# Optimization experiments

Hardware: AMD Instinct MI355X
Metric: run time of the kernel (lower is better)

The kernel has to match this reference:

```python
import jax, jax.numpy as jnp
import numpy as np

# static config (mirrors params)
T, B, NA, NF = 48, 256, 23, 4
D = NA * NF          # y_dim = 92
XD = 2               # x_dim
H = 128              # rnn_dim
HD = 128             # h_dim
NL = 2               # n_layers
FS = 0.1
BURN = 12
IN_ENC = XD + D + H  # GRU input size = 222
A0, A1 = 12, 11      # agents 0..11 -> net0, 12..22 -> net1


def setup_inputs() -> dict:
    key = jax.random.key(0)
    ks = jax.random.split(key, 16)
    s = 0.05
    rn = lambda k, shape: jax.random.normal(k, shape, jnp.float32) * s
    return {
        "states": jax.random.normal(ks[0], (T + 1, 1, B, D), jnp.float32),
        # per-network (leading dim 2) GRU layer-0 and layer-1 weights (torch GRU layout: [r|z|n])
        "W_ih0": rn(ks[1], (2, 3 * H, IN_ENC)),
        "W_hh0": rn(ks[2], (2, 3 * H, H)),
        "b_ih0": rn(ks[3], (2, 3 * H)),
        "b_hh0": rn(ks[4], (2, 3 * H)),
        "W_ih1": rn(ks[5], (2, 3 * H, H)),
        "W_hh1": rn(ks[6], (2, 3 * H, H)),
        "b_ih1": rn(ks[7], (2, 3 * H)),
        "b_hh1": rn(ks[8], (2, 3 * H)),
        # decoder MLP (dropout is identity in eval) + mean head
        "W1": rn(ks[9], (2, HD, H)),
        "b1": rn(ks[10], (2, HD)),
        "W2": rn(ks[11], (2, HD, HD)),
        "b2": rn(ks[12], (2, HD)),
        "Wm": rn(ks[13], (2, XD, HD)),
        "bm": rn(ks[14], (2, XD)),
        "rollout": 0,
        "train": 0,
    }


def _gru_cell(x, h, Wih, Whh, bih, bhh):
    gi = x @ Wih.T + bih
    gh = h @ Whh.T + bhh
    r = jax.nn.sigmoid(gi[:, :H] + gh[:, :H])
    z = jax.nn.sigmoid(gi[:, H:2 * H] + gh[:, H:2 * H])
    n = jnp.tanh(gi[:, 2 * H:] + r * gh[:, 2 * H:])
    return (1.0 - z) * n + z * h


def _batch_error(a, b):
    # sum over batch of the euclidean norm over features
    return jnp.sum(jnp.sqrt(jnp.sum((a - b) ** 2, axis=1)))


def _group_step(h, y_t, y3, y3n, lo, hi, g, P):
    # h: [NL, A*B, H]; agents lo..hi-1 of network g, folded into the batch dim
    A = hi - lo
    vel = y3[:, lo:hi, 2:4].transpose(1, 0, 2).reshape(A * B, 2)
    pos = y3[:, lo:hi, 0:2].transpose(1, 0, 2).reshape(A * B, 2)
    vel_true = y3n[:, lo:hi, 2:4].transpose(1, 0, 2).reshape(A * B, 2)
    pos_true = y3n[:, lo:hi, 0:2].transpose(1, 0, 2).reshape(A * B, 2)
    y_rep = jnp.broadcast_to(y_t[None], (A, B, D)).reshape(A * B, D)
    h_last = h[-1]
    enc_in = jnp.concatenate([vel, y_rep, h_last], axis=1)  # [A*B, IN_ENC]
    # decoder uses the PRE-update hidden state
    d = jax.nn.relu(h_last @ P["W1"][g].T + P["b1"][g])
    d = jax.nn.relu(d @ P["W2"][g].T + P["b2"][g])
    dm = d @ P["Wm"][g].T + P["bm"][g]  # [A*B, XD]
    # 2-layer GRU step
    h0n = _gru_cell(enc_in, h[0], P["W_ih0"][g], P["W_hh0"][g], P["b_ih0"][g], P["b_hh0"][g])
    h1n = _gru_cell(h0n, h[1], P["W_ih1"][g], P["W_hh1"][g], P["b_ih1"][g], P["b_hh1"][g])
    h_new = jnp.stack([h0n, h1n])
    L = _batch_error(dm, vel_true)
    ep = _batch_error(pos + vel * FS, pos_true)
    ev = _batch_error(dm[:, :2], vel_true)
    return h_new, L, ep, ev


def _forward(states, P):
    y_seq = states[:T, 0]       # [T, B, D]
    y_next = states[1:T + 1, 0]  # [T, B, D]

    def step(carry, xs):
        h0, h1, L, ep, ev = carry
        y_t, y_t1, t = xs
        y3 = y_t.reshape(B, NA, NF)
        y3n = y_t1.reshape(B, NA, NF)
        h0n, L0, ep0, ev0 = _group_step(h0, y_t, y3, y3n, 0, A0, 0, P)
        h1n, L1, ep1, ev1 = _group_step(h1, y_t, y3, y3n, A0, NA, 1, P)
        m = (t >= BURN).astype(jnp.float32)
        return (h0n, h1n, L + L0 + L1, ep + m * (ep0 + ep1), ev + m * (ev0 + ev1)), None

    init = (jnp.zeros((NL, A0 * B, H), jnp.float32),
            jnp.zeros((NL, A1 * B, H), jnp.float32),
            jnp.zeros((), jnp.float32), jnp.zeros((), jnp.float32), jnp.zeros((), jnp.float32))
    (h0, h1, L, ep, ev), _ = jax.lax.scan(step, init, (y_seq, y_next, jnp.arange(T)))
    L_rec = L / (T * NA)
    e_pos = ep / ((T - BURN) * NA)
    e_vel = ev / ((T - BURN) * NA)
    return L_rec, e_pos, e_vel


def reference(states, W_ih0, W_hh0, b_ih0, b_hh0, W_ih1, W_hh1, b_ih1, b_hh1,
              W1, b1, W2, b2, Wm, bm, rollout, train):
    P = dict(W_ih0=W_ih0, W_hh0=W_hh0, b_ih0=b_ih0, b_hh0=b_hh0,
             W_ih1=W_ih1, W_hh1=W_hh1, b_ih1=b_ih1, b_hh1=b_hh1,
             W1=W1, b1=b1, W2=W2, b2=b2, Wm=Wm, bm=bm)
    return _forward(states, P)
```

## Files before the change

kernel.cpp:

```cpp
#include <hip/hip_runtime.h>
#include <hip/hip_bf16.h>


typedef unsigned short u16;
typedef unsigned int u32;
typedef unsigned char u8;
typedef __attribute__((ext_vector_type(4))) float f32x4;
typedef __attribute__((ext_vector_type(4))) int i32x4;
typedef __attribute__((ext_vector_type(8))) int i32x8;

#define MFMA128(acc, a, b) \
  (acc) = __builtin_amdgcn_mfma_scale_f32_16x16x128_f8f6f4( \
      (a), (b), (acc), 0, 0, 0, 0x7F7F7F7F, 0, 0x7F7F7F7F)

__device__ __forceinline__ i32x8 ld8(const u8* p) { return *(const i32x8*)p; }
__device__ __forceinline__ void pinV(i32x8& x) { asm volatile("" : "+v"(x)); }

__device__ __forceinline__ u8 f2e4(float v) {
  return (u8)(__builtin_amdgcn_cvt_pk_fp8_f32(v, 0.f, 0, false) & 0xff);
}
__device__ __forceinline__ u32 pk4(float a, float b, float c, float d) {
  u32 p = (u32)__builtin_amdgcn_cvt_pk_fp8_f32(a, b, 0, false);
  return (u32)__builtin_amdgcn_cvt_pk_fp8_f32(c, d, (int)p, true);
}
__device__ __forceinline__ float sigf(float x) {
  return __builtin_amdgcn_rcpf(1.f + __expf(-x));
}
__device__ __forceinline__ float tanh_fast(float x) {
  return 1.f - 2.f * __builtin_amdgcn_rcpf(1.f + __expf(2.f * x));
}

__device__ __forceinline__ int swzo(int row, int o) {
  return (row << 7) + ((((o >> 5) ^ row) & 3) << 5) +
         ((((o >> 4) ^ (row >> 2)) & 1) << 4) + (o & 15);
}
__device__ __forceinline__ i32x8 ldfrag(const u8* b, int row, int kq) {
  const int h = (row >> 2) & 1;
  const int a = (row << 7) + (((kq ^ row) & 3) << 5);
  i32x4 lo = *(const i32x4*)(b + a + (h << 4));
  i32x4 hi = *(const i32x4*)(b + a + ((h ^ 1) << 4));
  return __builtin_shufflevector(lo, hi, 0, 1, 2, 3, 4, 5, 6, 7);
}

constexpr int E0 = 2 * 384 * 352;
constexpr int E1 = E0 + 2 * 384 * 256;
constexpr int E2 = E1 + 2 * 128 * 128;
constexpr int E3 = E2 + 2 * 128 * 128;
constexpr int E4 = E3 + 2 * 128 * 128;
constexpr int E5 = E4 + 2 * 128 * 128;
constexpr int NBIAS = 2048;
constexpr int TOTAL = E5 + NBIAS + 4;
constexpr int WB_BYTE_OFF = 16384;

constexpr int WB0A_REL = E5;
constexpr int YBG2_REL = WB0A_REL + 23 * 384 * 128;
constexpr int NA1 = TOTAL;
constexpr int NA2 = NA1 + 23 * 384 * 128;
constexpr int NA3 = NA2 + 48 * 256 * 128;

__global__ void prep_kernel(const float* __restrict__ states,
                            const float* __restrict__ Wih0, const float* __restrict__ Whh0,
                            const float* __restrict__ bih0, const float* __restrict__ bhh0,
                            const float* __restrict__ Wih1, const float* __restrict__ Whh1,
                            const float* __restrict__ bih1, const float* __restrict__ bhh1,
                            const float* __restrict__ W1, const float* __restrict__ W2,
                            u8* __restrict__ wb, float* __restrict__ wsf) {
  for (int idx = blockIdx.x * blockDim.x + threadIdx.x; idx < NA3;
       idx += gridDim.x * blockDim.x) {
    if (idx < E0) {
      int g = idx / 135168;
      int r = idx - g * 135168;
      int j = r / 352;
      int k = r - j * 352;
      const float* wi = Wih0 + (g * 384 + j) * 222;
      float v;
      if (k < 94) v = wi[k];
      else if (k < 96) v = 0.f;
      else if (k < 224) v = wi[k - 2];
      else v = Whh0[(g * 384 + j) * 128 + (k - 224)];
      wb[idx] = f2e4(v);
    } else if (idx < E1) {
      int q = idx - E0;
      int g = q / 98304;
      int r = q - g * 98304;
      int j = r >> 8;
      int k = r & 255;
      float v = (k < 128) ? Wih1[(g * 384 + j) * 128 + k]
                          : Whh1[(g * 384 + j) * 128 + (k - 128)];
      wb[idx] = f2e4(v);
    } else if (idx < E2) {
      int q = idx - E1; int g = q >> 14; int r = q & 16383; int j = r >> 7; int k = r & 127;
      wb[idx] = f2e4(W1[(g * 128 + j) * 128 + k]);
    } else if (idx < E3) {
      int q = idx - E2; int g = q >> 14; int r = q & 16383; int j = r >> 7; int k = r & 127;
      wb[idx] = f2e4(W2[(g * 128 + j) * 128 + k]);
    } else if (idx < E5) {
      wb[idx] = 0;
    } else if (idx < E5 + NBIAS) {
      int q = idx - E5;
      float v;
      if (q < 512)       { int g = q >> 8, j = q & 255;              v = bih0[g*384 + j] + bhh0[g*384 + j]; }
      else if (q < 768)  { int p = q - 512;  int g = p >> 7, j = p & 127; v = bih0[g*384 + 256 + j]; }
      else if (q < 1024) { int p = q - 768;  int g = p >> 7, j = p & 127; v = bhh0[g*384 + 256 + j]; }
      else if (q < 1536) { int p = q - 1024; int g = p >> 8, j = p & 255; v = bih1[g*384 + j] + bhh1[g*384 + j]; }
      else if (q < 1792) { int p = q - 1536; int g = p >> 7, j = p & 127; v = bih1[g*384 + 256 + j]; }
      else               { int p = q - 1792; int g = p >> 7, j = p & 127; v = bhh1[g*384 + 256 + j]; }
      wsf[4 + q] = v;
    } else if (idx < TOTAL) {
      wsf[idx - (E5 + NBIAS)] = 0.f;
    } else if (idx < NA2) {
      int q = idx - NA1;
      int a = q / 49152;
      int r = q - a * 49152;
      int j = r >> 7;
      int k = r & 127;
      const float* wi = Wih0 + (((a >= 12) ? 1 : 0) * 384 + j) * 222;
      float v = (k < 92) ? wi[2 + k] : 0.f;
      if (k == a * 4 + 2) v += wi[0];
      if (k == a * 4 + 3) v += wi[1];
      wb[WB0A_REL + q] = f2e4(v);
    } else {
      int q = idx - NA2;
      int t = q >> 15;
      int r = q & 32767;
      int row = r >> 7;
      int k = r & 127;
      float v = (k < 92) ? states[((size_t)t * 256 + row) * 92 + k] : 0.f;
      wb[YBG2_REL + q] = f2e4(v);
    }
  }
}

__global__ __launch_bounds__(512, 2) __attribute__((amdgpu_waves_per_eu(2, 2)))
void rnn_kernel(const float* __restrict__ states,
                const u8* __restrict__ wb,
                float* __restrict__ wsf,
                const float* __restrict__ b1g,
                const float* __restrict__ b2g,
                const float* __restrict__ Wmg,
                const float* __restrict__ bmg) {
  const int blk = blockIdx.x;
  const int g = (blk < 96) ? 0 : 1;
  const int r0 = (g == 0) ? (blk * 32) : ((blk - 96) * 32);
  const int aAg = (g == 0 ? 0 : 12) + (r0 >> 8);
  const int b0 = r0 & 255;

  const int tid = threadIdx.x;
  const int wid = tid >> 6;
  const int ln = tid & 63;
  const int j_in = ln & 15;
  const int kq = ln >> 4;
  const int c0 = wid * 16 + kq * 4;
  const int jh = wid * 16 + j_in;

  __shared__ __align__(64) u8 h0b[2][32 * 128];
  __shared__ __align__(64) u8 h1b[2][32 * 128];
  __shared__ __align__(64) u8 d1b[32 * 128];
  __shared__ __align__(64) u8 d2b[32 * 128];
  __shared__ __align__(16) float bias[1536];
  __shared__ float dmv[48][32][2];
  __shared__ float red[8][3];

  const u8* W0   = wb + g * 135168;
  const u8* W1c  = wb + E0 + g * 98304;
  const u8* Wm1p = wb + E1 + g * 16384;
  const u8* Wm2p = wb + E2 + g * 16384;
  const u8* WB0A = wb + WB0A_REL + aAg * 49152;
  const u8* YBG  = wb + YBG2_REL;

  i32x8 w0r0 = ld8(WB0A + jh * 128 + kq * 32);
  i32x8 w0r1 = ld8(W0 + jh * 352 + 96 + kq * 32);
  i32x8 w0r2 = ld8(W0 + jh * 352 + 224 + kq * 32);
  i32x8 w0z0 = ld8(WB0A + (128 + jh) * 128 + kq * 32);
  i32x8 w0z1 = ld8(W0 + (128 + jh) * 352 + 96 + kq * 32);
  i32x8 w0z2 = ld8(W0 + (128 + jh) * 352 + 224 + kq * 32);
  i32x8 w0n0 = ld8(WB0A + (256 + jh) * 128 + kq * 32);
  i32x8 w0n1 = ld8(W0 + (256 + jh) * 352 + 96 + kq * 32);
  i32x8 wn0  = ld8(W0 + (256 + jh) * 352 + 224 + kq * 32);
  i32x8 w1r0 = ld8(W1c + jh * 256 + kq * 32);
  i32x8 w1r1 = ld8(W1c + jh * 256 + 128 + kq * 32);
  i32x8 w1z0 = ld8(W1c + (128 + jh) * 256 + kq * 32);
  i32x8 w1z1 = ld8(W1c + (128 + jh) * 256 + 128 + kq * 32);
  i32x8 w1n0 = ld8(W1c + (256 + jh) * 256 + kq * 32);
  i32x8 wn1  = ld8(W1c + (256 + jh) * 256 + 128 + kq * 32);
  i32x8 wm1  = ld8(Wm1p + jh * 128 + kq * 32);
  i32x8 wm2  = ld8(Wm2p + jh * 128 + kq * 32);
  pinV(w0r0); pinV(w0r1); pinV(w0r2);
  pinV(w0z0); pinV(w0z1); pinV(w0z2);
  pinV(w0n0); pinV(w0n1); pinV(wn0);
  pinV(w1r0); pinV(w1r1); pinV(w1z0); pinV(w1z1);
  pinV(w1n0); pinV(wn1); pinV(wm1); pinV(wm2);

  for (int i = tid; i < 1536; i += 512) {
    float v;
    if (i < 256)       v = wsf[4 + g * 256 + i];
    else if (i < 384)  v = wsf[516 + g * 128 + (i - 256)];
    else if (i < 512)  v = wsf[772 + g * 128 + (i - 384)];
    else if (i < 768)  v = wsf[1028 + g * 256 + (i - 512)];
    else if (i < 896)  v = wsf[1540 + g * 128 + (i - 768)];
    else if (i < 1024) v = wsf[1796 + g * 128 + (i - 896)];
    else if (i < 1152) v = b1g[g * 128 + (i - 1024)];
    else if (i < 1280) v = b2g[g * 128 + (i - 1152)];
    else               v = Wmg[g * 256 + (i - 1280)];
    bias[i] = v;
  }
  for (int i = tid; i < 32 * 128; i += 512) { h0b[0][i] = 0; h1b[0][i] = 0; }

  f32x4 hv0[2] = {{0,0,0,0},{0,0,0,0}};
  f32x4 hv1[2] = {{0,0,0,0},{0,0,0,0}};
  __syncthreads();

  for (int t = 0; t < 48; ++t) {
    const int cur = t & 1, nxt = cur ^ 1;
    const u8* h0c = h0b[cur]; u8* h0n = h0b[nxt];
    const u8* h1c = h1b[cur]; u8* h1n = h1b[nxt];
    const u8* yt = YBG + t * 32768;

    i32x8 fh1k[2];
    {
      f32x4 b1v = *(const f32x4*)(bias + 1024 + c0);
      f32x4 brv = *(const f32x4*)(bias + c0);
      f32x4 bzv = *(const f32x4*)(bias + 128 + c0);
      f32x4 biv = *(const f32x4*)(bias + 256 + c0);
      f32x4 bhv = *(const f32x4*)(bias + 384 + c0);
#pragma unroll
      for (int nt = 0; nt < 2; ++nt) {
        const int row = nt * 16 + j_in;
        i32x8 fy  = ld8(yt + (b0 + row) * 128 + kq * 32);
        i32x8 fh1 = ldfrag(h1c, row, kq);
        i32x8 fh0 = ldfrag(h0c, row, kq);
        fh1k[nt] = fh1;
        f32x4 mm = {0,0,0,0};
        MFMA128(mm, wm1, fh1);
        f32x4 aR = {0,0,0,0}, aZ = {0,0,0,0}, aN = {0,0,0,0}, aG = {0,0,0,0};
        MFMA128(aR, w0r0, fy);  MFMA128(aZ, w0z0, fy);  MFMA128(aN, w0n0, fy);
        MFMA128(aR, w0r1, fh1); MFMA128(aZ, w0z1, fh1); MFMA128(aN, w0n1, fh1);
        MFMA128(aR, w0r2, fh0); MFMA128(aZ, w0z2, fh0); MFMA128(aG, wn0, fh0);
        *(u32*)(d1b + swzo(row, c0)) =
          pk4(fmaxf(mm[0]+b1v[0],0.f), fmaxf(mm[1]+b1v[1],0.f),
              fmaxf(mm[2]+b1v[2],0.f), fmaxf(mm[3]+b1v[3],0.f));
#pragma unroll
        for (int i = 0; i < 4; ++i) {
          float rv = sigf(aR[i] + brv[i]);
          float zv = sigf(aZ[i] + bzv[i]);
          float nv = tanh_fast(aN[i] + biv[i] + rv * (aG[i] + bhv[i]));
          hv0[nt][i] = (1.f - zv) * nv + zv * hv0[nt][i];
        }
        *(u32*)(h0n + swzo(row, c0)) = pk4(hv0[nt][0], hv0[nt][1], hv0[nt][2], hv0[nt][3]);
      }
    }
    if (t > 0) {
      int row = tid >> 4, c = (tid >> 3) & 1, part = tid & 7;
      const float* wmr = bias + 1280 + c * 128 + part * 16;
      float s = 0.f;
#pragma unroll
      for (int q = 0; q < 4; ++q) {
        u32 w = *(const u32*)(d2b + swzo(row, part * 16 + q * 4));
        s += wmr[q * 4 + 0] * __builtin_amdgcn_cvt_f32_fp8((int)w, 0);
        s += wmr[q * 4 + 1] * __builtin_amdgcn_cvt_f32_fp8((int)w, 1);
        s += wmr[q * 4 + 2] * __builtin_amdgcn_cvt_f32_fp8((int)w, 2);
        s += wmr[q * 4 + 3] * __builtin_amdgcn_cvt_f32_fp8((int)w, 3);
      }
      s += __shfl_xor(s, 1); s += __shfl_xor(s, 2); s += __shfl_xor(s, 4);
      if (part == 0) dmv[t - 1][row][c] = s;
    }
    __syncthreads();

    {
      f32x4 b2v = *(const f32x4*)(bias + 1152 + c0);
      f32x4 brv = *(const f32x4*)(bias + 512 + c0);
      f32x4 bzv = *(const f32x4*)(bias + 640 + c0);
      f32x4 biv = *(const f32x4*)(bias + 768 + c0);
      f32x4 bhv = *(const f32x4*)(bias + 896 + c0);
#pragma unroll
      for (int nt = 0; nt < 2; ++nt) {
        const int row = nt * 16 + j_in;
        i32x8 fd1 = ldfrag(d1b, row, kq);
        i32x8 fg0 = ldfrag(h0n, row, kq);
        f32x4 mm = {0,0,0,0};
        MFMA128(mm, wm2, fd1);
        f32x4 aR = {0,0,0,0}, aZ = {0,0,0,0}, aN = {0,0,0,0}, aG = {0,0,0,0};
        MFMA128(aR, w1r0, fg0);      MFMA128(aZ, w1z0, fg0);      MFMA128(aN, w1n0, fg0);
        MFMA128(aR, w1r1, fh1k[nt]); MFMA128(aZ, w1z1, fh1k[nt]); MFMA128(aG, wn1, fh1k[nt]);
        *(u32*)(d2b + swzo(row, c0)) =
          pk4(fmaxf(mm[0]+b2v[0],0.f), fmaxf(mm[1]+b2v[1],0.f),
              fmaxf(mm[2]+b2v[2],0.f), fmaxf(mm[3]+b2v[3],0.f));
#pragma unroll
        for (int i = 0; i < 4; ++i) {
          float rv = sigf(aR[i] + brv[i]);
          float zv = sigf(aZ[i] + bzv[i]);
          float nv = tanh_fast(aN[i] + biv[i] + rv * (aG[i] + bhv[i]));
          hv1[nt][i] = (1.f - zv) * nv + zv * hv1[nt][i];
        }
        *(u32*)(h1n + swzo(row, c0)) = pk4(hv1[nt][0], hv1[nt][1], hv1[nt][2], hv1[nt][3]);
      }
    }
    __syncthreads();
  }

  {
    int row = tid >> 4, c = (tid >> 3) & 1, part = tid & 7;
    const float* wmr = bias + 1280 + c * 128 + part * 16;
    float s = 0.f;
#pragma unroll
    for (int q = 0; q < 4; ++q) {
      u32 w = *(const u32*)(d2b + swzo(row, part * 16 + q * 4));
      s += wmr[q * 4 + 0] * __builtin_amdgcn_cvt_f32_fp8((int)w, 0);
      s += wmr[q * 4 + 1] * __builtin_amdgcn_cvt_f32_fp8((int)w, 1);
      s += wmr[q * 4 + 2] * __builtin_amdgcn_cvt_f32_fp8((int)w, 2);
      s += wmr[q * 4 + 3] * __builtin_amdgcn_cvt_f32_fp8((int)w, 3);
    }
    s += __shfl_xor(s, 1); s += __shfl_xor(s, 2); s += __shfl_xor(s, 4);
    if (part == 0) dmv[47][row][c] = s;
  }
  __syncthreads();

  float accL = 0.f, accEp = 0.f, accEv = 0.f;
  const float bm0 = bmg[g * 2], bm1 = bmg[g * 2 + 1];
  for (int idx = tid; idx < 1536; idx += 512) {
    int t = idx >> 5, row = idx & 31;
    const float* sr = states + ((size_t)(t * 256 + b0 + row)) * 92 + aAg * 4;
    const float* sn = sr + 256 * 92;
    float dx = dmv[t][row][0] + bm0 - sn[2];
    float dy = dmv[t][row][1] + bm1 - sn[3];
    float e = sqrtf(dx * dx + dy * dy);
    accL += e;
    if (t >= 12) {
      accEv += e;
      float ex = sr[0] + 0.1f * sr[2] - sn[0];
      float ey = sr[1] + 0.1f * sr[3] - sn[1];
      accEp += sqrtf(ex * ex + ey * ey);
    }
  }
#pragma unroll
  for (int k = 1; k < 64; k <<= 1) {
    accL  += __shfl_xor(accL, k);
    accEp += __shfl_xor(accEp, k);
    accEv += __shfl_xor(accEv, k);
  }
  if (ln == 0) { red[wid][0] = accL; red[wid][1] = accEp; red[wid][2] = accEv; }
  __syncthreads();
  if (tid < 3) {
    float s = 0.f;
    for (int i = 0; i < 8; ++i) s += red[i][tid];
    atomicAdd(&wsf[tid], s);
  }
}

__global__ void fin_kernel(const float* __restrict__ wacc, float* __restrict__ out) {
  if (threadIdx.x == 0 && blockIdx.x == 0) {
    out[0] = wacc[0] / 1104.f;
    out[1] = wacc[1] / 828.f;
    out[2] = wacc[2] / 828.f;
  }
}

extern "C" void kernel_launch(void* const* d_in, const int* in_sizes, int n_in,
                              void* d_out, int out_size, void* d_ws, size_t ws_size,
                              hipStream_t stream) {
  const float* states = (const float*)d_in[0];
  const float* Wih0 = (const float*)d_in[1];
  const float* Whh0 = (const float*)d_in[2];
  const float* bih0 = (const float*)d_in[3];
  const float* bhh0 = (const float*)d_in[4];
  const float* Wih1 = (const float*)d_in[5];
  const float* Whh1 = (const float*)d_in[6];
  const float* bih1 = (const float*)d_in[7];
  const float* bhh1 = (const float*)d_in[8];
  const float* W1   = (const float*)d_in[9];
  const float* b1   = (const float*)d_in[10];
  const float* W2   = (const float*)d_in[11];
  const float* b2   = (const float*)d_in[12];
  const float* Wm   = (const float*)d_in[13];
  const float* bm   = (const float*)d_in[14];

  float* wsf = (float*)d_ws;
  u8* wb = (u8*)d_ws + WB_BYTE_OFF;

  int prep_blocks = (NA3 + 255) / 256;
  if (prep_blocks > 2048) prep_blocks = 2048;
  prep_kernel<<<prep_blocks, 256, 0, stream>>>(states, Wih0, Whh0, bih0, bhh0,
                                               Wih1, Whh1, bih1, bhh1,
                                               W1, W2, wb, wsf);
  rnn_kernel<<<184, 512, 0, stream>>>(states, wb, wsf, b1, b2, Wm, bm);
  fin_kernel<<<1, 64, 0, stream>>>(wsf, (float*)d_out);
}
```

Before: 274.9 us.

## Halve rows per block to double grid size for the sequential RNN

Each block now processes 16 batch rows instead of 32, so the grid doubles from 184 to 368 blocks and each wave handles one 16-row MFMA tile per step instead of two. The goal is to shorten the serial 48-step critical path per block and fill more CUs, because the recurrence cannot be parallelised over time. The cost is that every block reloads the full register-resident weight set, and with the occupancy hint raised to 4 waves per EU the register budget per thread shrinks, which may force spills. The decoder-head reduction and loss loop are re-indexed to match the 16-row tile.

```diff
diff --git a/kernel.cpp b/kernel.cpp
--- a/kernel.cpp
+++ b/kernel.cpp
@@ -131,7 +131,7 @@
   }
 }
 
-__global__ __launch_bounds__(512, 2) __attribute__((amdgpu_waves_per_eu(2, 2)))
+__global__ __launch_bounds__(512) __attribute__((amdgpu_waves_per_eu(4, 4)))
 void rnn_kernel(const float* __restrict__ states,
                 const u8* __restrict__ wb,
                 float* __restrict__ wsf,
@@ -140,8 +140,8 @@
                 const float* __restrict__ Wmg,
                 const float* __restrict__ bmg) {
   const int blk = blockIdx.x;
-  const int g = (blk < 96) ? 0 : 1;
-  const int r0 = (g == 0) ? (blk * 32) : ((blk - 96) * 32);
+  const int g = (blk < 192) ? 0 : 1;
+  const int r0 = (g == 0) ? (blk * 16) : ((blk - 192) * 16);
   const int aAg = (g == 0 ? 0 : 12) + (r0 >> 8);
   const int b0 = r0 & 255;
 
@@ -153,12 +153,12 @@
   const int c0 = wid * 16 + kq * 4;
   const int jh = wid * 16 + j_in;
 
-  __shared__ __align__(64) u8 h0b[2][32 * 128];
-  __shared__ __align__(64) u8 h1b[2][32 * 128];
-  __shared__ __align__(64) u8 d1b[32 * 128];
-  __shared__ __align__(64) u8 d2b[32 * 128];
+  __shared__ __align__(64) u8 h0b[2][16 * 128];
+  __shared__ __align__(64) u8 h1b[2][16 * 128];
+  __shared__ __align__(64) u8 d1b[16 * 128];
+  __shared__ __align__(64) u8 d2b[16 * 128];
   __shared__ __align__(16) float bias[1536];
-  __shared__ float dmv[48][32][2];
+  __shared__ float dmv[48][16][2];
   __shared__ float red[8][3];
 
   const u8* W0   = wb + g * 135168;
@@ -204,65 +204,63 @@
     else               v = Wmg[g * 256 + (i - 1280)];
     bias[i] = v;
   }
-  for (int i = tid; i < 32 * 128; i += 512) { h0b[0][i] = 0; h1b[0][i] = 0; }
-
-  f32x4 hv0[2] = {{0,0,0,0},{0,0,0,0}};
-  f32x4 hv1[2] = {{0,0,0,0},{0,0,0,0}};
+  for (int i = tid; i < 16 * 128; i += 512) { h0b[0][i] = 0; h1b[0][i] = 0; }
+
+  f32x4 hv0 = {0,0,0,0};
+  f32x4 hv1 = {0,0,0,0};
   __syncthreads();
 
+  const int row = j_in;
   for (int t = 0; t < 48; ++t) {
     const int cur = t & 1, nxt = cur ^ 1;
     const u8* h0c = h0b[cur]; u8* h0n = h0b[nxt];
     const u8* h1c = h1b[cur]; u8* h1n = h1b[nxt];
     const u8* yt = YBG + t * 32768;
 
-    i32x8 fh1k[2];
+    i32x8 fh1k;
     {
       f32x4 b1v = *(const f32x4*)(bias + 1024 + c0);
       f32x4 brv = *(const f32x4*)(bias + c0);
       f32x4 bzv = *(const f32x4*)(bias + 128 + c0);
       f32x4 biv = *(const f32x4*)(bias + 256 + c0);
       f32x4 bhv = *(const f32x4*)(bias + 384 + c0);
-#pragma unroll
-      for (int nt = 0; nt < 2; ++nt) {
-        const int row = nt * 16 + j_in;
-        i32x8 fy  = ld8(yt + (b0 + row) * 128 + kq * 32);
-        i32x8 fh1 = ldfrag(h1c, row, kq);
-        i32x8 fh0 = ldfrag(h0c, row, kq);
-        fh1k[nt] = fh1;
-        f32x4 mm = {0,0,0,0};
-        MFMA128(mm, wm1, fh1);
-        f32x4 aR = {0,0,0,0}, aZ = {0,0,0,0}, aN = {0,0,0,0}, aG = {0,0,0,0};
-        MFMA128(aR, w0r0, fy);  MFMA128(aZ, w0z0, fy);  MFMA128(aN, w0n0, fy);
-        MFMA128(aR, w0r1, fh1); MFMA128(aZ, w0z1, fh1); MFMA128(aN, w0n1, fh1);
-        MFMA128(aR, w0r2, fh0); MFMA128(aZ, w0z2, fh0); MFMA128(aG, wn0, fh0);
-        *(u32*)(d1b + swzo(row, c0)) =
-          pk4(fmaxf(mm[0]+b1v[0],0.f), fmaxf(mm[1]+b1v[1],0.f),
-              fmaxf(mm[2]+b1v[2],0.f), fmaxf(mm[3]+b1v[3],0.f));
-#pragma unroll
-        for (int i = 0; i < 4; ++i) {
-          float rv = sigf(aR[i] + brv[i]);
-          float zv = sigf(aZ[i] + bzv[i]);
-          float nv = tanh_fast(aN[i] + biv[i] + rv * (aG[i] + bhv[i]));
-          hv0[nt][i] = (1.f - zv) * nv + zv * hv0[nt][i];
-        }
-        *(u32*)(h0n + swzo(row, c0)) = pk4(hv0[nt][0], hv0[nt][1], hv0[nt][2], hv0[nt][3]);
+      i32x8 fy  = ld8(yt + (b0 + row) * 128 + kq * 32);
+      i32x8 fh1 = ldfrag(h1c, row, kq);
+      i32x8 fh0 = ldfrag(h0c, row, kq);
+      fh1k = fh1;
+      f32x4 mm = {0,0,0,0};
+      MFMA128(mm, wm1, fh1);
+      f32x4 aR = {0,0,0,0}, aZ = {0,0,0,0}, aN = {0,0,0,0}, aG = {0,0,0,0};
+      MFMA128(aR, w0r0, fy);  MFMA128(aZ, w0z0, fy);  MFMA128(aN, w0n0, fy);
+      MFMA128(aR, w0r1, fh1); MFMA128(aZ, w0z1, fh1); MFMA128(aN, w0n1, fh1);
+      MFMA128(aR, w0r2, fh0); MFMA128(aZ, w0z2, fh0); MFMA128(aG, wn0, fh0);
+      *(u32*)(d1b + swzo(row, c0)) =
+        pk4(fmaxf(mm[0]+b1v[0],0.f), fmaxf(mm[1]+b1v[1],0.f),
+            fmaxf(mm[2]+b1v[2],0.f), fmaxf(mm[3]+b1v[3],0.f));
+#pragma unroll
+      for (int i = 0; i < 4; ++i) {
+        float rv = sigf(aR[i] + brv[i]);
+        float zv = sigf(aZ[i] + bzv[i]);
+        float nv = tanh_fast(aN[i] + biv[i] + rv * (aG[i] + bhv[i]));
+        hv0[i] = (1.f - zv) * nv + zv * hv0[i];
       }
+      *(u32*)(h0n + swzo(row, c0)) = pk4(hv0[0], hv0[1], hv0[2], hv0[3]);
     }
     if (t > 0) {
-      int row = tid >> 4, c = (tid >> 3) & 1, part = tid & 7;
-      const float* wmr = bias + 1280 + c * 128 + part * 16;
+      int drow = tid >> 5, c = (tid >> 4) & 1, part = tid & 15;
+      const float* wmr = bias + 1280 + c * 128 + part * 8;
       float s = 0.f;
 #pragma unroll
-      for (int q = 0; q < 4; ++q) {
-        u32 w = *(const u32*)(d2b + swzo(row, part * 16 + q * 4));
+      for (int q = 0; q < 2; ++q) {
+        u32 w = *(const u32*)(d2b + swzo(drow, part * 8 + q * 4));
         s += wmr[q * 4 + 0] * __builtin_amdgcn_cvt_f32_fp8((int)w, 0);
         s += wmr[q * 4 + 1] * __builtin_amdgcn_cvt_f32_fp8((int)w, 1);
         s += wmr[q * 4 + 2] * __builtin_amdgcn_cvt_f32_fp8((int)w, 2);
         s += wmr[q * 4 + 3] * __builtin_amdgcn_cvt_f32_fp8((int)w, 3);
       }
-      s += __shfl_xor(s, 1); s += __shfl_xor(s, 2); s += __shfl_xor(s, 4);
-      if (part == 0) dmv[t - 1][row][c] = s;
+      s += __shfl_xor(s, 1); s += __shfl_xor(s, 2);
+      s += __shfl_xor(s, 4); s += __shfl_xor(s, 8);
+      if (part == 0) dmv[t - 1][drow][c] = s;
     }
     __syncthreads();
 
@@ -272,57 +270,54 @@
       f32x4 bzv = *(const f32x4*)(bias + 640 + c0);
       f32x4 biv = *(const f32x4*)(bias + 768 + c0);
       f32x4 bhv = *(const f32x4*)(bias + 896 + c0);
-#pragma unroll
-      for (int nt = 0; nt < 2; ++nt) {
-        const int row = nt * 16 + j_in;
-        i32x8 fd1 = ldfrag(d1b, row, kq);
-        i32x8 fg0 = ldfrag(h0n, row, kq);
-        f32x4 mm = {0,0,0,0};
-        MFMA128(mm, wm2, fd1);
-        f32x4 aR = {0,0,0,0}, aZ = {0,0,0,0}, aN = {0,0,0,0}, aG = {0,0,0,0};
-        MFMA128(aR, w1r0, fg0);      MFMA128(aZ, w1z0, fg0);      MFMA128(aN, w1n0, fg0);
-        MFMA128(aR, w1r1, fh1k[nt]); MFMA128(aZ, w1z1, fh1k[nt]); MFMA128(aG, wn1, fh1k[nt]);
-        *(u32*)(d2b + swzo(row, c0)) =
-          pk4(fmaxf(mm[0]+b2v[0],0.f), fmaxf(mm[1]+b2v[1],0.f),
-              fmaxf(mm[2]+b2v[2],0.f), fmaxf(mm[3]+b2v[3],0.f));
-#pragma unroll
-        for (int i = 0; i < 4; ++i) {
-          float rv = sigf(aR[i] + brv[i]);
-          float zv = sigf(aZ[i] + bzv[i]);
-          float nv = tanh_fast(aN[i] + biv[i] + rv * (aG[i] + bhv[i]));
-          hv1[nt][i] = (1.f - zv) * nv + zv * hv1[nt][i];
-        }
-        *(u32*)(h1n + swzo(row, c0)) = pk4(hv1[nt][0], hv1[nt][1], hv1[nt][2], hv1[nt][3]);
+      i32x8 fd1 = ldfrag(d1b, row, kq);
+      i32x8 fg0 = ldfrag(h0n, row, kq);
+      f32x4 mm = {0,0,0,0};
+      MFMA128(mm, wm2, fd1);
+      f32x4 aR = {0,0,0,0}, aZ = {0,0,0,0}, aN = {0,0,0,0}, aG = {0,0,0,0};
+      MFMA128(aR, w1r0, fg0);   MFMA128(aZ, w1z0, fg0);   MFMA128(aN, w1n0, fg0);
+      MFMA128(aR, w1r1, fh1k);  MFMA128(aZ, w1z1, fh1k);  MFMA128(aG, wn1, fh1k);
+      *(u32*)(d2b + swzo(row, c0)) =
+        pk4(fmaxf(mm[0]+b2v[0],0.f), fmaxf(mm[1]+b2v[1],0.f),
+            fmaxf(mm[2]+b2v[2],0.f), fmaxf(mm[3]+b2v[3],0.f));
+#pragma unroll
+      for (int i = 0; i < 4; ++i) {
+        float rv = sigf(aR[i] + brv[i]);
+        float zv = sigf(aZ[i] + bzv[i]);
+        float nv = tanh_fast(aN[i] + biv[i] + rv * (aG[i] + bhv[i]));
+        hv1[i] = (1.f - zv) * nv + zv * hv1[i];
       }
+      *(u32*)(h1n + swzo(row, c0)) = pk4(hv1[0], hv1[1], hv1[2], hv1[3]);
     }
     __syncthreads();
   }
 
   {
-    int row = tid >> 4, c = (tid >> 3) & 1, part = tid & 7;
-    const float* wmr = bias + 1280 + c * 128 + part * 16;
+    int drow = tid >> 5, c = (tid >> 4) & 1, part = tid & 15;
+    const float* wmr = bias + 1280 + c * 128 + part * 8;
     float s = 0.f;
 #pragma unroll
-    for (int q = 0; q < 4; ++q) {
-      u32 w = *(const u32*)(d2b + swzo(row, part * 16 + q * 4));
+    for (int q = 0; q < 2; ++q) {
+      u32 w = *(const u32*)(d2b + swzo(drow, part * 8 + q * 4));
       s += wmr[q * 4 + 0] * __builtin_amdgcn_cvt_f32_fp8((int)w, 0);
       s += wmr[q * 4 + 1] * __builtin_amdgcn_cvt_f32_fp8((int)w, 1);
       s += wmr[q * 4 + 2] * __builtin_amdgcn_cvt_f32_fp8((int)w, 2);
       s += wmr[q * 4 + 3] * __builtin_amdgcn_cvt_f32_fp8((int)w, 3);
     }
-    s += __shfl_xor(s, 1); s += __shfl_xor(s, 2); s += __shfl_xor(s, 4);
-    if (part == 0) dmv[47][row][c] = s;
+    s += __shfl_xor(s, 1); s += __shfl_xor(s, 2);
+    s += __shfl_xor(s, 4); s += __shfl_xor(s, 8);
+    if (part == 0) dmv[47][drow][c] = s;
   }
   __syncthreads();
 
   float accL = 0.f, accEp = 0.f, accEv = 0.f;
   const float bm0 = bmg[g * 2], bm1 = bmg[g * 2 + 1];
-  for (int idx = tid; idx < 1536; idx += 512) {
-    int t = idx >> 5, row = idx & 31;
-    const float* sr = states + ((size_t)(t * 256 + b0 + row)) * 92 + aAg * 4;
+  for (int idx = tid; idx < 768; idx += 512) {
+    int t = idx >> 4, rr = idx & 15;
+    const float* sr = states + ((size_t)(t * 256 + b0 + rr)) * 92 + aAg * 4;
     const float* sn = sr + 256 * 92;
-    float dx = dmv[t][row][0] + bm0 - sn[2];
-    float dy = dmv[t][row][1] + bm1 - sn[3];
+    float dx = dmv[t][rr][0] + bm0 - sn[2];
+    float dy = dmv[t][rr][1] + bm1 - sn[3];
     float e = sqrtf(dx * dx + dy * dy);
     accL += e;
     if (t >= 12) {
@@ -382,6 +377,6 @@
   prep_kernel<<<prep_blocks, 256, 0, stream>>>(states, Wih0, Whh0, bih0, bhh0,
                                                Wih1, Whh1, bih1, bhh1,
                                                W1, W2, wb, wsf);
-  rnn_kernel<<<184, 512, 0, stream>>>(states, wb, wsf, b1, b2, Wm, bm);
+  rnn_kernel<<<368, 512, 0, stream>>>(states, wb, wsf, b1, b2, Wm, bm);
   fin_kernel<<<1, 64, 0, stream>>>(wsf, (float*)d_out);
 }
```

New measurement: 722.7 us. 163% more time.

## Stagger wave tile order, prioritize MFMA issue, and fuse final normalization kernel

Applied to the files above, without the earlier changes.

Alternates the order of the two row tiles between odd and even waves and raises wave priority around the MFMA sequences, so matrix and transcendental work from different waves overlap. The MFMAs are reordered and the decoder-head reduction is moved ahead of phase 1. The separate finalize kernel is replaced by a last-block atomic counter that writes the normalized outputs, removing one launch. The counter depends on the workspace slot being zeroed by the prep kernel, and the added fence and atomic add a small tail cost.

```diff
diff --git a/kernel.cpp b/kernel.cpp
--- a/kernel.cpp
+++ b/kernel.cpp
@@ -138,7 +138,8 @@
                 const float* __restrict__ b1g,
                 const float* __restrict__ b2g,
                 const float* __restrict__ Wmg,
-                const float* __restrict__ bmg) {
+                const float* __restrict__ bmg,
+                float* __restrict__ out) {
   const int blk = blockIdx.x;
   const int g = (blk < 96) ? 0 : 1;
   const int r0 = (g == 0) ? (blk * 32) : ((blk - 96) * 32);
@@ -210,45 +211,14 @@
   f32x4 hv1[2] = {{0,0,0,0},{0,0,0,0}};
   __syncthreads();
 
+  const int wodd = wid & 1;
+
   for (int t = 0; t < 48; ++t) {
     const int cur = t & 1, nxt = cur ^ 1;
     const u8* h0c = h0b[cur]; u8* h0n = h0b[nxt];
     const u8* h1c = h1b[cur]; u8* h1n = h1b[nxt];
     const u8* yt = YBG + t * 32768;
 
-    i32x8 fh1k[2];
-    {
-      f32x4 b1v = *(const f32x4*)(bias + 1024 + c0);
-      f32x4 brv = *(const f32x4*)(bias + c0);
-      f32x4 bzv = *(const f32x4*)(bias + 128 + c0);
-      f32x4 biv = *(const f32x4*)(bias + 256 + c0);
-      f32x4 bhv = *(const f32x4*)(bias + 384 + c0);
-#pragma unroll
-      for (int nt = 0; nt < 2; ++nt) {
-        const int row = nt * 16 + j_in;
-        i32x8 fy  = ld8(yt + (b0 + row) * 128 + kq * 32);
-        i32x8 fh1 = ldfrag(h1c, row, kq);
-        i32x8 fh0 = ldfrag(h0c, row, kq);
-        fh1k[nt] = fh1;
-        f32x4 mm = {0,0,0,0};
-        MFMA128(mm, wm1, fh1);
-        f32x4 aR = {0,0,0,0}, aZ = {0,0,0,0}, aN = {0,0,0,0}, aG = {0,0,0,0};
-        MFMA128(aR, w0r0, fy);  MFMA128(aZ, w0z0, fy);  MFMA128(aN, w0n0, fy);
-        MFMA128(aR, w0r1, fh1); MFMA128(aZ, w0z1, fh1); MFMA128(aN, w0n1, fh1);
-        MFMA128(aR, w0r2, fh0); MFMA128(aZ, w0z2, fh0); MFMA128(aG, wn0, fh0);
-        *(u32*)(d1b + swzo(row, c0)) =
-          pk4(fmaxf(mm[0]+b1v[0],0.f), fmaxf(mm[1]+b1v[1],0.f),
-              fmaxf(mm[2]+b1v[2],0.f), fmaxf(mm[3]+b1v[3],0.f));
-#pragma unroll
-        for (int i = 0; i < 4; ++i) {
-          float rv = sigf(aR[i] + brv[i]);
-          float zv = sigf(aZ[i] + bzv[i]);
-          float nv = tanh_fast(aN[i] + biv[i] + rv * (aG[i] + bhv[i]));
-          hv0[nt][i] = (1.f - zv) * nv + zv * hv0[nt][i];
-        }
-        *(u32*)(h0n + swzo(row, c0)) = pk4(hv0[nt][0], hv0[nt][1], hv0[nt][2], hv0[nt][3]);
-      }
-    }
     if (t > 0) {
       int row = tid >> 4, c = (tid >> 3) & 1, part = tid & 7;
       const float* wmr = bias + 1280 + c * 128 + part * 16;
@@ -264,6 +234,46 @@
       s += __shfl_xor(s, 1); s += __shfl_xor(s, 2); s += __shfl_xor(s, 4);
       if (part == 0) dmv[t - 1][row][c] = s;
     }
+
+    i32x8 fh1k0, fh1k1;
+    {
+      f32x4 b1v = *(const f32x4*)(bias + 1024 + c0);
+      f32x4 brv = *(const f32x4*)(bias + c0);
+      f32x4 bzv = *(const f32x4*)(bias + 128 + c0);
+      f32x4 biv = *(const f32x4*)(bias + 256 + c0);
+      f32x4 bhv = *(const f32x4*)(bias + 384 + c0);
+#define P1BODY(NT, FH1K)                                                     \
+      {                                                                      \
+        const int row = (NT) * 16 + j_in;                                    \
+        i32x8 fy  = ld8(yt + (b0 + row) * 128 + kq * 32);                    \
+        i32x8 fh1 = ldfrag(h1c, row, kq);                                    \
+        i32x8 fh0 = ldfrag(h0c, row, kq);                                    \
+        FH1K = fh1;                                                          \
+        f32x4 mm = {0,0,0,0};                                                \
+        f32x4 aR = {0,0,0,0}, aZ = {0,0,0,0}, aN = {0,0,0,0}, aG = {0,0,0,0};\
+        __builtin_amdgcn_s_setprio(1);                                       \
+        MFMA128(mm, wm1, fh1);                                               \
+        MFMA128(aR, w0r1, fh1); MFMA128(aZ, w0z1, fh1); MFMA128(aN, w0n1, fh1);\
+        MFMA128(aR, w0r2, fh0); MFMA128(aZ, w0z2, fh0); MFMA128(aG, wn0, fh0);\
+        MFMA128(aR, w0r0, fy);  MFMA128(aZ, w0z0, fy);  MFMA128(aN, w0n0, fy);\
+        __builtin_amdgcn_s_setprio(0);                                       \
+        *(u32*)(d1b + swzo(row, c0)) =                                       \
+          pk4(fmaxf(mm[0]+b1v[0],0.f), fmaxf(mm[1]+b1v[1],0.f),              \
+              fmaxf(mm[2]+b1v[2],0.f), fmaxf(mm[3]+b1v[3],0.f));             \
+        _Pragma("unroll")                                                    \
+        for (int i = 0; i < 4; ++i) {                                        \
+          float rv = sigf(aR[i] + brv[i]);                                   \
+          float zv = sigf(aZ[i] + bzv[i]);                                   \
+          float nv = tanh_fast(aN[i] + biv[i] + rv * (aG[i] + bhv[i]));      \
+          hv0[NT][i] = (1.f - zv) * nv + zv * hv0[NT][i];                    \
+        }                                                                    \
+        *(u32*)(h0n + swzo(row, c0)) =                                       \
+          pk4(hv0[NT][0], hv0[NT][1], hv0[NT][2], hv0[NT][3]);               \
+      }
+      if (wodd) { P1BODY(1, fh1k1) P1BODY(0, fh1k0) }
+      else      { P1BODY(0, fh1k0) P1BODY(1, fh1k1) }
+#undef P1BODY
+    }
     __syncthreads();
 
     {
@@ -272,28 +282,34 @@
       f32x4 bzv = *(const f32x4*)(bias + 640 + c0);
       f32x4 biv = *(const f32x4*)(bias + 768 + c0);
       f32x4 bhv = *(const f32x4*)(bias + 896 + c0);
-#pragma unroll
-      for (int nt = 0; nt < 2; ++nt) {
-        const int row = nt * 16 + j_in;
-        i32x8 fd1 = ldfrag(d1b, row, kq);
-        i32x8 fg0 = ldfrag(h0n, row, kq);
-        f32x4 mm = {0,0,0,0};
-        MFMA128(mm, wm2, fd1);
-        f32x4 aR = {0,0,0,0}, aZ = {0,0,0,0}, aN = {0,0,0,0}, aG = {0,0,0,0};
-        MFMA128(aR, w1r0, fg0);      MFMA128(aZ, w1z0, fg0);      MFMA128(aN, w1n0, fg0);
-        MFMA128(aR, w1r1, fh1k[nt]); MFMA128(aZ, w1z1, fh1k[nt]); MFMA128(aG, wn1, fh1k[nt]);
-        *(u32*)(d2b + swzo(row, c0)) =
-          pk4(fmaxf(mm[0]+b2v[0],0.f), fmaxf(mm[1]+b2v[1],0.f),
-              fmaxf(mm[2]+b2v[2],0.f), fmaxf(mm[3]+b2v[3],0.f));
-#pragma unroll
-        for (int i = 0; i < 4; ++i) {
-          float rv = sigf(aR[i] + brv[i]);
-          float zv = sigf(aZ[i] + bzv[i]);
-          float nv = tanh_fast(aN[i] + biv[i] + rv * (aG[i] + bhv[i]));
-          hv1[nt][i] = (1.f - zv) * nv + zv * hv1[nt][i];
-        }
-        *(u32*)(h1n + swzo(row, c0)) = pk4(hv1[nt][0], hv1[nt][1], hv1[nt][2], hv1[nt][3]);
+#define P2BODY(NT, FH1K)                                                     \
+      {                                                                      \
+        const int row = (NT) * 16 + j_in;                                    \
+        i32x8 fd1 = ldfrag(d1b, row, kq);                                    \
+        i32x8 fg0 = ldfrag(h0n, row, kq);                                    \
+        f32x4 mm = {0,0,0,0};                                                \
+        f32x4 aR = {0,0,0,0}, aZ = {0,0,0,0}, aN = {0,0,0,0}, aG = {0,0,0,0};\
+        __builtin_amdgcn_s_setprio(1);                                       \
+        MFMA128(aR, w1r1, FH1K); MFMA128(aZ, w1z1, FH1K); MFMA128(aG, wn1, FH1K);\
+        MFMA128(mm, wm2, fd1);                                               \
+        MFMA128(aR, w1r0, fg0);  MFMA128(aZ, w1z0, fg0);  MFMA128(aN, w1n0, fg0);\
+        __builtin_amdgcn_s_setprio(0);                                       \
+        *(u32*)(d2b + swzo(row, c0)) =                                       \
+          pk4(fmaxf(mm[0]+b2v[0],0.f), fmaxf(mm[1]+b2v[1],0.f),              \
+              fmaxf(mm[2]+b2v[2],0.f), fmaxf(mm[3]+b2v[3],0.f));             \
+        _Pragma("unroll")                                                    \
+        for (int i = 0; i < 4; ++i) {                                        \
+          float rv = sigf(aR[i] + brv[i]);                                   \
+          float zv = sigf(aZ[i] + bzv[i]);                                   \
+          float nv = tanh_fast(aN[i] + biv[i] + rv * (aG[i] + bhv[i]));      \
+          hv1[NT][i] = (1.f - zv) * nv + zv * hv1[NT][i];                    \
+        }                                                                    \
+        *(u32*)(h1n + swzo(row, c0)) =                                       \
+          pk4(hv1[NT][0], hv1[NT][1], hv1[NT][2], hv1[NT][3]);               \
       }
+      if (wodd) { P2BODY(1, fh1k1) P2BODY(0, fh1k0) }
+      else      { P2BODY(0, fh1k0) P2BODY(1, fh1k1) }
+#undef P2BODY
     }
     __syncthreads();
   }
@@ -345,13 +361,19 @@
     for (int i = 0; i < 8; ++i) s += red[i][tid];
     atomicAdd(&wsf[tid], s);
   }
-}
-
-__global__ void fin_kernel(const float* __restrict__ wacc, float* __restrict__ out) {
-  if (threadIdx.x == 0 && blockIdx.x == 0) {
-    out[0] = wacc[0] / 1104.f;
-    out[1] = wacc[1] / 828.f;
-    out[2] = wacc[2] / 828.f;
+
+  __threadfence();
+  __syncthreads();
+  if (tid == 0) {
+    int old = atomicAdd((int*)&wsf[3], 1);
+    if (old == 183) {
+      float L  = atomicAdd(&wsf[0], 0.f);
+      float Ep = atomicAdd(&wsf[1], 0.f);
+      float Ev = atomicAdd(&wsf[2], 0.f);
+      out[0] = L / 1104.f;
+      out[1] = Ep / 828.f;
+      out[2] = Ev / 828.f;
+    }
   }
 }
 
@@ -382,6 +404,6 @@
   prep_kernel<<<prep_blocks, 256, 0, stream>>>(states, Wih0, Whh0, bih0, bhh0,
                                                Wih1, Whh1, bih1, bhh1,
                                                W1, W2, wb, wsf);
-  rnn_kernel<<<184, 512, 0, stream>>>(states, wb, wsf, b1, b2, Wm, bm);
-  fin_kernel<<<1, 64, 0, stream>>>(wsf, (float*)d_out);
-}
+  rnn_kernel<<<184, 512, 0, stream>>>(states, wb, wsf, b1, b2, Wm, bm,
+                                      (float*)d_out);
+}
```

After: 491.5 us. 1.79x slower.
